# Kernel tuning notes

Measured on AMD Instinct MI355X. Metric: run time of the kernel, lower is better.

Reference implementation:

```python
import jax, jax.numpy as jnp
import numpy as np
from jax import lax

TAU, H1, H2 = 0.25, 1.0, 1.0

def make_stencil_weight():
    # depthwise OIHW weight (2,1,3,3): 5-point explicit diffusion stencil
    hx = TAU / (H1 * H1)
    hy = TAU / (H2 * H2)
    w = np.zeros((2, 1, 3, 3), dtype=np.float32)
    for c in range(2):
        w[c, 0, 1, 0] = hx
        w[c, 0, 1, 2] = hx
        w[c, 0, 0, 1] = hy
        w[c, 0, 2, 1] = hy
        w[c, 0, 1, 1] = 1.0 - 2.0 * hx - 2.0 * hy
    return jnp.asarray(w)

def setup_inputs() -> dict:
    key = jax.random.key(0)
    x = jax.random.normal(key, (16, 2, 1024, 1024), dtype=jnp.float32)
    return {"x": x, "weight": make_stencil_weight(), "time_steps": 20}

def reference(x, weight, time_steps):
    def step(h, _):
        hp = jnp.pad(h, ((0, 0), (0, 0), (1, 1), (1, 1)), mode="reflect")
        h = lax.conv_general_dilated(
            hp, weight, window_strides=(1, 1), padding="VALID",
            dimension_numbers=("NCHW", "OIHW", "NCHW"),
            feature_group_count=2)
        return h, None
    out, _ = lax.scan(step, x, None, length=time_steps)
    return out
```

## Files before the change

### kernel.cpp

```cpp
#include <hip/hip_runtime.h>


#define IMG  1024
#define KF   10
#define RB   64
#define SW   232
#define NSW  5
#define LPAD 12
#define NB   (IMG/RB)
#define NPL  32
#define WPL  (NB*NSW)
#define NWAVES (NPL*WPL)

__device__ __forceinline__ float dpp_left(float v) {
    return __int_as_float(__builtin_amdgcn_update_dpp(
        __float_as_int(v), __float_as_int(v), 0x138, 0xf, 0xf, false));
}
__device__ __forceinline__ float dpp_right(float v) {
    return __int_as_float(__builtin_amdgcn_update_dpp(
        __float_as_int(v), __float_as_int(v), 0x130, 0xf, 0xf, false));
}

#define STAGE(jj, OV, NV, GEN)                                               \
    {                                                                        \
        float4 Cn; bool pr = true;                                           \
        const int f = _r - (jj);                                             \
        bool act = true;                                                     \
        if (GEN) {                                                           \
            const int lo = max(ob - KF + (jj), 0);                           \
            const int hi = min(ob + RB - 1 + KF - (jj), IMG - 1);            \
            act = (f >= lo) && (f <= hi);                                    \
        }                                                                    \
        if (act) {                                                           \
            const float4 mid = NV;                                           \
            float4 vs;                                                       \
            if (GEN && f == 0) {                       \
                vs.x = C.x + C.x; vs.y = C.y + C.y;                          \
                vs.z = C.z + C.z; vs.w = C.w + C.w;                          \
            } else if (GEN && f == IMG - 1) {    \
                vs.x = OV.x + OV.x; vs.y = OV.y + OV.y;                      \
                vs.z = OV.z + OV.z; vs.w = OV.w + OV.w;                      \
            } else {                                                         \
                vs.x = OV.x + C.x; vs.y = OV.y + C.y;                        \
                vs.z = OV.z + C.z; vs.w = OV.w + C.w;                        \
            }                                                                \
            float lf = dpp_left(mid.w);                                      \
            float rg = dpp_right(mid.x);                                     \
            if (is_cL) lf = mid.y;                  \
            if (is_cR) rg = mid.z;                \
            Cn.x = vs.x*w01 + (lf    + mid.y)*w10 + mid.x*w11;               \
            Cn.y = vs.y*w01 + (mid.x + mid.z)*w10 + mid.y*w11;               \
            Cn.z = vs.z*w01 + (mid.y + mid.w)*w10 + mid.z*w11;               \
            Cn.w = vs.w*w01 + (mid.z + rg   )*w10 + mid.w*w11;               \
        } else { pr = false; Cn = C; }                                       \
        if (prod) { OV = C; }                                                \
        C = Cn; prod = GEN ? pr : true;                                      \
    }

#define STEPN(rv, PF, GEN, O0,N0,O1,N1,O2,N2,O3,N3,O4,N4,                    \
                           O5,N5,O6,N6,O7,N7,O8,N8,O9,N9)                    \
    do {                                                                     \
        const int _r = (rv);                                                 \
        float4 C = PF;                                                       \
        if (_r + 2 <= in_hi)                                                 \
            PF = *(const float4*)(lp + (size_t)(_r + 2) * IMG);              \
        bool prod = GEN ? (_r <= in_hi) : true;                              \
        STAGE(1,  O0, N0, GEN)                                               \
        STAGE(2,  O1, N1, GEN)                                               \
        STAGE(3,  O2, N2, GEN)                                               \
        STAGE(4,  O3, N3, GEN)                                               \
        STAGE(5,  O4, N4, GEN)                                               \
        STAGE(6,  O5, N5, GEN)                                               \
        STAGE(7,  O6, N6, GEN)                                               \
        STAGE(8,  O7, N7, GEN)                                               \
        STAGE(9,  O8, N8, GEN)                                               \
        STAGE(10, O9, N9, GEN)                                               \
        if ((!GEN || prod) && st_ok)                                         \
            *(float4*)(op + (size_t)(_r - KF) * IMG) = C;                    \
    } while (0)

#define STEP_E(rv, GEN) STEPN(rv, p0, GEN, a0,b0,a1,b1,a2,b2,a3,b3,a4,b4,    \
                                           a5,b5,a6,b6,a7,b7,a8,b8,a9,b9)
#define STEP_O(rv, GEN) STEPN(rv, p1, GEN, b0,a0,b1,a1,b2,a2,b3,a3,b4,a4,    \
                                           b5,a5,b6,a6,b7,a7,b8,a8,b9,a9)

__global__ __launch_bounds__(64, 3) void diff10(
    const float* __restrict__ src, float* __restrict__ dst,
    const float* __restrict__ wt)
{
    const int lane  = threadIdx.x;
    const int gw    = blockIdx.x;
    const int plane = gw / WPL;
    const int rem   = gw - plane * WPL;
    const int band  = rem / NSW;
    const int sw    = rem - band * NSW;

    const int ob  = band * RB;
    const int uc0 = sw * SW;
    const int c0  = uc0 - LPAD + 4 * lane;
    const int cld = min(max(c0, 0), IMG - 4);

    const float* __restrict__ lp = src + (size_t)plane * IMG * IMG + cld;
    float* __restrict__       op = dst + (size_t)plane * IMG * IMG + cld;

    const float* w9 = wt + (size_t)(plane & 1) * 9;
    const float w01 = w9[1];
    const float w10 = w9[3];
    const float w11 = w9[4];

    const bool is_cL  = (c0 == 0);
    const bool is_cR  = (c0 == IMG - 4);
    const bool st_ok  = (c0 >= uc0) && (c0 < uc0 + SW) && (c0 <= IMG - 4);

    const int r_lo  = max(ob - KF, 0);
    const int in_hi = min(ob + RB - 1 + KF, IMG - 1);
    const int r_hi  = ob + RB - 1 + KF;
    const int head_end = r_lo + 2 * KF - 1;
    const int st_end   = min(r_hi, IMG - 1);

    float4 a0{}, a1{}, a2{}, a3{}, a4{}, a5{}, a6{}, a7{}, a8{}, a9{};
    float4 b0{}, b1{}, b2{}, b3{}, b4{}, b5{}, b6{}, b7{}, b8{}, b9{};

    float4 p0, p1;
    p0 = *(const float4*)(lp + (size_t)r_lo * IMG);
    p1 = (r_lo + 1 <= in_hi) ? *(const float4*)(lp + (size_t)(r_lo + 1) * IMG) : p0;

    for (int r = r_lo; r <= head_end; r += 2) {
        STEP_E(r,     1);
        STEP_O(r + 1, 1);
    }
    for (int r = head_end + 1; r <= st_end; r += 2) {
        STEP_E(r,     0);
        STEP_O(r + 1, 0);
    }
    for (int r = st_end + 1; r <= r_hi; r += 2) {
        STEP_E(r,     1);
        STEP_O(r + 1, 1);
    }
}

extern "C" void kernel_launch(void* const* d_in, const int* in_sizes, int n_in,
                              void* d_out, int out_size, void* d_ws, size_t ws_size,
                              hipStream_t stream) {
    const float* x  = (const float*)d_in[0];
    const float* wt = (const float*)d_in[1];
    float* out = (float*)d_out;
    float* ws  = (float*)d_ws;

    dim3 g(NWAVES), b(64);
    diff10<<<g, b, 0, stream>>>(x,  ws,  wt);
    diff10<<<g, b, 0, stream>>>(ws, out, wt);
}
```

Before: 393.7 us.

## Fuse all twenty diffusion steps into one temporally blocked kernel pass

Doubles the temporal fusion depth from 10 to 20 stages so a single kernel launch computes all time steps. This removes the workspace round trip and the second launch, halving global memory traffic. In exchange the column halo grows (LPAD 20, so fewer useful columns per wave) and register pressure doubles with 40 float4 row buffers, which lowers occupancy to 2 waves per SIMD. It also switches to packed float2 vector math and disables loop unrolling to contain code size.

```diff
diff --git a/kernel.cpp b/kernel.cpp
--- a/kernel.cpp
+++ b/kernel.cpp
@@ -2,15 +2,18 @@
 
 
 #define IMG  1024
-#define KF   10
+#define KF   20
 #define RB   64
-#define SW   232
+#define LPAD 20
+#define SW   216
 #define NSW  5
-#define LPAD 12
 #define NB   (IMG/RB)
 #define NPL  32
 #define WPL  (NB*NSW)
 #define NWAVES (NPL*WPL)
+
+typedef float f32x4 __attribute__((ext_vector_type(4)));
+typedef float f32x2 __attribute__((ext_vector_type(2)));
 
 __device__ __forceinline__ float dpp_left(float v) {
     return __int_as_float(__builtin_amdgcn_update_dpp(
@@ -23,7 +26,7 @@
 
 #define STAGE(jj, OV, NV, GEN)                                               \
     {                                                                        \
-        float4 Cn; bool pr = true;                                           \
+        f32x4 Cn; bool pr = true;                                            \
         const int f = _r - (jj);                                             \
         bool act = true;                                                     \
         if (GEN) {                                                           \
@@ -32,59 +35,69 @@
             act = (f >= lo) && (f <= hi);                                    \
         }                                                                    \
         if (act) {                                                           \
-            const float4 mid = NV;                                           \
-            float4 vs;                                                       \
-            if (GEN && f == 0) {                       \
-                vs.x = C.x + C.x; vs.y = C.y + C.y;                          \
-                vs.z = C.z + C.z; vs.w = C.w + C.w;                          \
-            } else if (GEN && f == IMG - 1) {    \
-                vs.x = OV.x + OV.x; vs.y = OV.y + OV.y;                      \
-                vs.z = OV.z + OV.z; vs.w = OV.w + OV.w;                      \
-            } else {                                                         \
-                vs.x = OV.x + C.x; vs.y = OV.y + C.y;                        \
-                vs.z = OV.z + C.z; vs.w = OV.w + C.w;                        \
-            }                                                                \
+            const f32x4 mid = NV;                                            \
+            f32x4 vs;                                                        \
+            if (GEN && f == 0)              vs = C + C;      \
+            else if (GEN && f == IMG - 1)   vs = OV + OV;   \
+            else                            vs = OV + C;                     \
             float lf = dpp_left(mid.w);                                      \
             float rg = dpp_right(mid.x);                                     \
             if (is_cL) lf = mid.y;                  \
             if (is_cR) rg = mid.z;                \
-            Cn.x = vs.x*w01 + (lf    + mid.y)*w10 + mid.x*w11;               \
-            Cn.y = vs.y*w01 + (mid.x + mid.z)*w10 + mid.y*w11;               \
-            Cn.z = vs.z*w01 + (mid.y + mid.w)*w10 + mid.z*w11;               \
-            Cn.w = vs.w*w01 + (mid.z + rg   )*w10 + mid.w*w11;               \
+            f32x2 hlo, hhi;                                                  \
+            hlo.x = lf    + mid.y;  hlo.y = mid.x + mid.z;                   \
+            hhi.x = mid.y + mid.w;  hhi.y = mid.z + rg;                      \
+            Cn.lo = vs.lo * w01 + hlo * w10 + mid.lo * w11;                  \
+            Cn.hi = vs.hi * w01 + hhi * w10 + mid.hi * w11;                  \
         } else { pr = false; Cn = C; }                                       \
         if (prod) { OV = C; }                                                \
         C = Cn; prod = GEN ? pr : true;                                      \
     }
 
-#define STEPN(rv, PF, GEN, O0,N0,O1,N1,O2,N2,O3,N3,O4,N4,                    \
-                           O5,N5,O6,N6,O7,N7,O8,N8,O9,N9)                    \
+#define STEPN(rv, PF, GEN,                                                   \
+              O0,N0,O1,N1,O2,N2,O3,N3,O4,N4,O5,N5,O6,N6,O7,N7,O8,N8,O9,N9,  \
+              O10,N10,O11,N11,O12,N12,O13,N13,O14,N14,O15,N15,O16,N16,      \
+              O17,N17,O18,N18,O19,N19)                                       \
     do {                                                                     \
         const int _r = (rv);                                                 \
-        float4 C = PF;                                                       \
+        f32x4 C = PF;                                                        \
         if (_r + 2 <= in_hi)                                                 \
-            PF = *(const float4*)(lp + (size_t)(_r + 2) * IMG);              \
+            PF = *(const f32x4*)(lp + (size_t)(_r + 2) * IMG);               \
         bool prod = GEN ? (_r <= in_hi) : true;                              \
-        STAGE(1,  O0, N0, GEN)                                               \
-        STAGE(2,  O1, N1, GEN)                                               \
-        STAGE(3,  O2, N2, GEN)                                               \
-        STAGE(4,  O3, N3, GEN)                                               \
-        STAGE(5,  O4, N4, GEN)                                               \
-        STAGE(6,  O5, N5, GEN)                                               \
-        STAGE(7,  O6, N6, GEN)                                               \
-        STAGE(8,  O7, N7, GEN)                                               \
-        STAGE(9,  O8, N8, GEN)                                               \
-        STAGE(10, O9, N9, GEN)                                               \
+        STAGE(1,  O0,  N0,  GEN)                                             \
+        STAGE(2,  O1,  N1,  GEN)                                             \
+        STAGE(3,  O2,  N2,  GEN)                                             \
+        STAGE(4,  O3,  N3,  GEN)                                             \
+        STAGE(5,  O4,  N4,  GEN)                                             \
+        STAGE(6,  O5,  N5,  GEN)                                             \
+        STAGE(7,  O6,  N6,  GEN)                                             \
+        STAGE(8,  O7,  N7,  GEN)                                             \
+        STAGE(9,  O8,  N8,  GEN)                                             \
+        STAGE(10, O9,  N9,  GEN)                                             \
+        STAGE(11, O10, N10, GEN)                                             \
+        STAGE(12, O11, N11, GEN)                                             \
+        STAGE(13, O12, N12, GEN)                                             \
+        STAGE(14, O13, N13, GEN)                                             \
+        STAGE(15, O14, N14, GEN)                                             \
+        STAGE(16, O15, N15, GEN)                                             \
+        STAGE(17, O16, N16, GEN)                                             \
+        STAGE(18, O17, N17, GEN)                                             \
+        STAGE(19, O18, N18, GEN)                                             \
+        STAGE(20, O19, N19, GEN)                                             \
         if ((!GEN || prod) && st_ok)                                         \
-            *(float4*)(op + (size_t)(_r - KF) * IMG) = C;                    \
+            *(f32x4*)(op + (size_t)(_r - KF) * IMG) = C;                     \
     } while (0)
 
-#define STEP_E(rv, GEN) STEPN(rv, p0, GEN, a0,b0,a1,b1,a2,b2,a3,b3,a4,b4,    \
-                                           a5,b5,a6,b6,a7,b7,a8,b8,a9,b9)
-#define STEP_O(rv, GEN) STEPN(rv, p1, GEN, b0,a0,b1,a1,b2,a2,b3,a3,b4,a4,    \
-                                           b5,a5,b6,a6,b7,a7,b8,a8,b9,a9)
+#define STEP_E(rv, GEN) STEPN(rv, p0, GEN,                                   \
+    a0,b0,a1,b1,a2,b2,a3,b3,a4,b4,a5,b5,a6,b6,a7,b7,a8,b8,a9,b9,             \
+    a10,b10,a11,b11,a12,b12,a13,b13,a14,b14,a15,b15,a16,b16,a17,b17,         \
+    a18,b18,a19,b19)
+#define STEP_O(rv, GEN) STEPN(rv, p1, GEN,                                   \
+    b0,a0,b1,a1,b2,a2,b3,a3,b4,a4,b5,a5,b6,a6,b7,a7,b8,a8,b9,a9,             \
+    b10,a10,b11,a11,b12,a12,b13,a13,b14,a14,b15,a15,b16,a16,b17,a17,         \
+    b18,a18,b19,a19)
 
-__global__ __launch_bounds__(64, 3) void diff10(
+__global__ __launch_bounds__(64, 2) void diff20(
     const float* __restrict__ src, float* __restrict__ dst,
     const float* __restrict__ wt)
 {
@@ -118,21 +131,26 @@
     const int head_end = r_lo + 2 * KF - 1;
     const int st_end   = min(r_hi, IMG - 1);
 
-    float4 a0{}, a1{}, a2{}, a3{}, a4{}, a5{}, a6{}, a7{}, a8{}, a9{};
-    float4 b0{}, b1{}, b2{}, b3{}, b4{}, b5{}, b6{}, b7{}, b8{}, b9{};
+    f32x4 a0=0,a1=0,a2=0,a3=0,a4=0,a5=0,a6=0,a7=0,a8=0,a9=0;
+    f32x4 a10=0,a11=0,a12=0,a13=0,a14=0,a15=0,a16=0,a17=0,a18=0,a19=0;
+    f32x4 b0=0,b1=0,b2=0,b3=0,b4=0,b5=0,b6=0,b7=0,b8=0,b9=0;
+    f32x4 b10=0,b11=0,b12=0,b13=0,b14=0,b15=0,b16=0,b17=0,b18=0,b19=0;
 
-    float4 p0, p1;
-    p0 = *(const float4*)(lp + (size_t)r_lo * IMG);
-    p1 = (r_lo + 1 <= in_hi) ? *(const float4*)(lp + (size_t)(r_lo + 1) * IMG) : p0;
+    f32x4 p0, p1;
+    p0 = *(const f32x4*)(lp + (size_t)r_lo * IMG);
+    p1 = *(const f32x4*)(lp + (size_t)(r_lo + 1) * IMG);
 
+    #pragma clang loop unroll(disable)
     for (int r = r_lo; r <= head_end; r += 2) {
         STEP_E(r,     1);
         STEP_O(r + 1, 1);
     }
+    #pragma clang loop unroll(disable)
     for (int r = head_end + 1; r <= st_end; r += 2) {
         STEP_E(r,     0);
         STEP_O(r + 1, 0);
     }
+    #pragma clang loop unroll(disable)
     for (int r = st_end + 1; r <= r_hi; r += 2) {
         STEP_E(r,     1);
         STEP_O(r + 1, 1);
@@ -145,9 +163,8 @@
     const float* x  = (const float*)d_in[0];
     const float* wt = (const float*)d_in[1];
     float* out = (float*)d_out;
-    float* ws  = (float*)d_ws;
+    (void)d_ws; (void)ws_size;
 
     dim3 g(NWAVES), b(64);
-    diff10<<<g, b, 0, stream>>>(x,  ws,  wt);
-    diff10<<<g, b, 0, stream>>>(ws, out, wt);
+    diff20<<<g, b, 0, stream>>>(x, out, wt);
 }
```

Measured after the change: 955.9 us. 143% more time.
